# Kernel tuning notes

Measured on AMD Instinct MI355X. Metric: run time of the kernel, lower is better.

The kernel has to match this reference:

```python
import jax, jax.numpy as jnp
import numpy as np
import math

B, S = 2, 2048
IN_FEATURES = 4096
OUT_FEATURES = 4096
BLOCK_SIZE = 64
NUM_FFT_MATRICES = 4
IN_BLOCKS = IN_FEATURES // BLOCK_SIZE
OUT_BLOCKS = OUT_FEATURES // BLOCK_SIZE  # 64


def setup_inputs() -> dict:
    key = jax.random.key(0)
    k1, k2 = jax.random.split(key)
    scale = 1.0 / math.sqrt(BLOCK_SIZE * IN_BLOCKS)
    x = jax.random.normal(k1, (B, S, IN_FEATURES), dtype=jnp.float32)
    circulant_params = jax.random.normal(
        k2, (NUM_FFT_MATRICES, OUT_BLOCKS, IN_BLOCKS, BLOCK_SIZE), dtype=jnp.float32) * scale
    channel_weights = jnp.ones((NUM_FFT_MATRICES,), dtype=jnp.float32) / NUM_FFT_MATRICES
    return {"x": x, "circulant_params": circulant_params, "channel_weights": channel_weights}


def reference(x, circulant_params, channel_weights):
    b, s, in_feat = x.shape
    # split channels into circulant blocks: (b, s, in_blocks, block)
    x_blocks = x.reshape(b, s, IN_BLOCKS, BLOCK_SIZE)
    x_fft = jnp.fft.rfft(x_blocks, axis=-1)                    # (b, s, i, F) complex
    circ_fft = jnp.fft.rfft(circulant_params, axis=-1)         # (m, o, i, F) complex
    # channel-weighted combine over the m fft matrices (linear, so fold into weights)
    circ_w = jnp.einsum('m,moif->oif', channel_weights.astype(circ_fft.dtype), circ_fft)
    # per-frequency complex contraction over in_blocks (the block-circulant matmul)
    y_fft = jnp.einsum('bsif,oif->bsof', x_fft, circ_w)        # (b, s, o, F)
    y = jnp.fft.irfft(y_fft, n=BLOCK_SIZE, axis=-1)            # (b, s, o, block)
    return y.reshape(b, s, OUT_FEATURES).astype(x.dtype)
```

## Files before the change

kernel.cpp:

```cpp
#include <hip/hip_runtime.h>
#include <math.h>


typedef unsigned short u16;
typedef unsigned int   u32;
typedef __attribute__((ext_vector_type(8))) short bf16x8;
typedef __attribute__((ext_vector_type(4))) float f32x4;

#define TWO_PI 6.2831853071795864769f
#define SLICE 262144u

#define XF_ELEMS (33u * 2u * SLICE)
#define BF_OFF   XF_ELEMS
#define BF_ELEMS (33u * 128u * 128u)
#define DT_OFF   (BF_OFF + BF_ELEMS)
#define DT_ELEMS (2u * 80u * 40u)
#define E_OFF    (DT_OFF + DT_ELEMS)
#define E_ELEMS  (64u * 3u * 40u)

__device__ __forceinline__ u16 f2bf(float f) {
    union { float f; unsigned u; } v; v.f = f;
    unsigned r = v.u + 0x7FFFu + ((v.u >> 16) & 1u);
    return (u16)(r >> 16);
}

__global__ void prep(const float* __restrict__ p, const float* __restrict__ cw,
                     u16* __restrict__ Bf, u16* __restrict__ Dt, u16* __restrict__ E) {
    const int tid = threadIdx.x;
    if (blockIdx.x == 0) {
        for (int e = tid; e < (int)DT_ELEMS; e += 256) {
            int kt = e / 3200, rem = e % 3200, n = rem / 40, kk = rem % 40;
            int k = kt * 32 + kk;
            float v = 0.f;
            if (n < 66 && kk < 32) {
                int f = n >> 1;
                float ang = TWO_PI * (float)((f * k) & 63) * (1.f / 64.f);
                v = (n & 1) ? -sinf(ang) : cosf(ang);
            }
            Dt[e] = f2bf(v);
        }
        for (int e = tid; e < (int)E_ELEMS; e += 256) {
            int t = e / 120, rem = e % 120, kt = rem / 40, kk = rem % 40;
            int k = kt * 32 + kk;
            float v = 0.f;
            if (k < 66 && kk < 32) {
                int f = k >> 1;
                float wf = (f == 0 || f == 32) ? 1.f : 2.f;
                float ang = TWO_PI * (float)((f * t) & 63) * (1.f / 64.f);
                v = (wf * (1.f / 64.f)) * ((k & 1) ? -sinf(ang) : cosf(ang));
            }
            E[e] = f2bf(v);
        }
        return;
    }
    __shared__ float  ct[4][64];
    __shared__ float2 trig[64];
    const int pr = tid >> 6, ln = tid & 63;
    if (tid < 64) {
        float s, c;
        sincosf(TWO_PI * (float)tid * (1.f / 64.f), &s, &c);
        trig[tid] = make_float2(s, c);
    }
    const int pg = (blockIdx.x - 1) * 4 + pr;
    const int o = pg >> 6, i = pg & 63;
    {
        const float* base = p + (size_t)o * 4096 + i * 64 + ln;
        ct[pr][ln] = cw[0] * base[0]      + cw[1] * base[262144]
                   + cw[2] * base[524288] + cw[3] * base[786432];
    }
    __syncthreads();
    if (ln < 33) {
        float cr = 0.f, ci = 0.f;
        for (int u = 0; u < 64; ++u) {
            float2 sc = trig[(ln * u) & 63];
            cr += ct[pr][u] * sc.y; ci -= ct[pr][u] * sc.x;
        }
        u16* b = Bf + (size_t)ln * 16384 + (2 * o) * 128 + 2 * i;
        b[0]   = f2bf(cr);  b[1]   = f2bf(-ci);
        b[128] = f2bf(ci);  b[129] = f2bf(cr);
    }
}

__global__ __launch_bounds__(256) void t1_dft(const float* __restrict__ x,
                                              const u16* __restrict__ Dt,
                                              u16* __restrict__ XF) {
    __shared__ u32 TR[33 * 4 * 68];
    const int tid = threadIdx.x, lane = tid & 63, wave = tid >> 6;
    const int lm = lane & 15, kq8 = (lane >> 4) * 8;
    const int blk = blockIdx.x;
    const float* xb = x + (size_t)blk * 16384;

    f32x4 acc[4][5];
#pragma unroll
    for (int mi = 0; mi < 4; ++mi)
#pragma unroll
        for (int ni = 0; ni < 5; ++ni) acc[mi][ni] = (f32x4){0.f, 0.f, 0.f, 0.f};

#pragma unroll
    for (int kt = 0; kt < 2; ++kt) {
        bf16x8 bfr[5];
#pragma unroll
        for (int ni = 0; ni < 5; ++ni)
            bfr[ni] = *(const bf16x8*)&Dt[(kt * 80 + ni * 16 + lm) * 40 + kq8];
#pragma unroll
        for (int mi = 0; mi < 4; ++mi) {
            const int row = wave * 64 + mi * 16 + lm;
            const float* rp = xb + row * 64 + kt * 32 + kq8;
            float4 p0 = *(const float4*)rp;
            float4 p1 = *(const float4*)(rp + 4);
            union { u16 u[8]; bf16x8 v; } pk;
            pk.u[0] = f2bf(p0.x); pk.u[1] = f2bf(p0.y);
            pk.u[2] = f2bf(p0.z); pk.u[3] = f2bf(p0.w);
            pk.u[4] = f2bf(p1.x); pk.u[5] = f2bf(p1.y);
            pk.u[6] = f2bf(p1.z); pk.u[7] = f2bf(p1.w);
#pragma unroll
            for (int ni = 0; ni < 5; ++ni)
                acc[mi][ni] = __builtin_amdgcn_mfma_f32_16x16x32_bf16(
                    pk.v, bfr[ni], acc[mi][ni], 0, 0, 0);
        }
    }

    const int r0 = (lane >> 4) * 4;
#pragma unroll
    for (int mi = 0; mi < 4; ++mi)
#pragma unroll
        for (int ni = 0; ni < 5; ++ni) {
            const int col = ni * 16 + lm;
            if (col < 66) {
                const int f = col >> 1, par = col & 1;
                const int rowb = wave * 64 + mi * 16 + r0;
                f32x4 v = acc[mi][ni];
#pragma unroll
                for (int r = 0; r < 4; ++r) {
                    int rr = rowb + r, tokl = rr >> 6, ii = rr & 63;
                    ((u16*)TR)[(f * 272 + tokl * 68 + ii) * 2 + par] = f2bf(v[r]);
                }
            }
        }
    __syncthreads();
    u32* XFu = (u32*)XF;
#pragma unroll
    for (int rnd = 0; rnd < 9; ++rnd) {
        int s = rnd * 16 + wave * 4 + (lane >> 4);
        if (s < 132) {
            int f = s >> 2, tokl = s & 3, c = lm * 4;
            uint4 v = *(const uint4*)&TR[f * 272 + tokl * 68 + c];
            *(uint4*)&XFu[(size_t)f * SLICE + (size_t)(blk * 4 + tokl) * 64 + c] = v;
        }
    }
}

#define GLD(g, l) __builtin_amdgcn_global_load_lds(                         \
        (const __attribute__((address_space(1))) void*)(g),                 \
        (__attribute__((address_space(3))) void*)(l), 16, 0, 0)

__global__ __launch_bounds__(256) void t2_freq(u16* __restrict__ XF,
                                               const u16* __restrict__ Bf) {
    __shared__ u16 sA[128 * 32];
    __shared__ u16 sB[128 * 32];
    const int f = blockIdx.y;
    u16* XFf = XF + (size_t)f * (2u * SLICE);
    const u16* Bff = Bf + (size_t)f * 16384;
    const int tid = threadIdx.x, lane = tid & 63, wid = tid >> 6;
    const int wm = wid >> 1, wn = wid & 1;
    const int lm = lane & 15, kq = (lane >> 4) * 8;
    const int tileM = blockIdx.x * 128;

    f32x4 acc[4][4];
#pragma unroll
    for (int i = 0; i < 4; ++i)
#pragma unroll
        for (int j = 0; j < 4; ++j) acc[i][j] = (f32x4){0.f, 0.f, 0.f, 0.f};

    const int e0 = tid * 8, e1 = 2048 + tid * 8;
    const u16* gA0 = XFf + (size_t)(tileM + (e0 >> 5)) * 128 + (e0 & 31);
    const u16* gA1 = XFf + (size_t)(tileM + (e1 >> 5)) * 128 + (e1 & 31);
    const u16* gB0 = Bff + (size_t)(e0 >> 5) * 128 + (e0 & 31);
    const u16* gB1 = Bff + (size_t)(e1 >> 5) * 128 + (e1 & 31);
    u16* lA0 = &sA[wid * 512];
    u16* lA1 = &sA[2048 + wid * 512];
    u16* lB0 = &sB[wid * 512];
    u16* lB1 = &sB[2048 + wid * 512];

#pragma unroll
    for (int kt = 0; kt < 128; kt += 32) {
        __syncthreads();
        GLD(gA0 + kt, lA0);
        GLD(gA1 + kt, lA1);
        GLD(gB0 + kt, lB0);
        GLD(gB1 + kt, lB1);
        __syncthreads();
        bf16x8 af[4], bfr[4];
#pragma unroll
        for (int mi = 0; mi < 4; ++mi)
            af[mi] = *(const bf16x8*)&sA[(wm * 64 + mi * 16 + lm) * 32 + kq];
#pragma unroll
        for (int ni = 0; ni < 4; ++ni)
            bfr[ni] = *(const bf16x8*)&sB[(wn * 64 + ni * 16 + lm) * 32 + kq];
#pragma unroll
        for (int mi = 0; mi < 4; ++mi)
#pragma unroll
            for (int ni = 0; ni < 4; ++ni)
                acc[mi][ni] = __builtin_amdgcn_mfma_f32_16x16x32_bf16(
                    af[mi], bfr[ni], acc[mi][ni], 0, 0, 0);
    }

    const int r0 = (lane >> 4) * 4;
#pragma unroll
    for (int mi = 0; mi < 4; ++mi)
#pragma unroll
        for (int ni = 0; ni < 4; ++ni) {
            const int row = tileM + wm * 64 + mi * 16 + r0;
            const int col = wn * 64 + ni * 16 + lm;
            f32x4 v = acc[mi][ni];
#pragma unroll
            for (int r = 0; r < 4; ++r)
                XFf[(size_t)(row + r) * 128 + col] = f2bf(v[r]);
        }
}

__global__ __launch_bounds__(256) void t3_idft(const u16* __restrict__ YF,
                                               const u16* __restrict__ E,
                                               float* __restrict__ y) {
    __shared__ u16 sA[3 * 128 * 40];
    __shared__ u16 sE[64 * 120];
    const int tid = threadIdx.x, lane = tid & 63, wave = tid >> 6;
    u32* sA32 = (u32*)sA;
#pragma unroll
    for (int j = 0; j < 4; ++j) {
        int e = j * 256 + tid;
        int kt = e >> 9, row = (e >> 2) & 127, w = e & 3;
        sA32[kt * 2560 + row * 20 + 8 + w] = 0u;
    }
#pragma unroll
    for (int j = 0; j < 10; ++j)
        sA32[5120 + j * 256 + tid] = 0u;
    {
        const u32* src = (const u32*)E;
#pragma unroll
        for (int j = 0; j < 15; ++j)
            ((u32*)sE)[j * 256 + tid] = src[j * 256 + tid];
    }
    __syncthreads();
    const int tok0 = blockIdx.x * 2;
    const u32* YFu = (const u32*)YF;
#pragma unroll
    for (int j = 0; j < 17; ++j) {
        int e = j * 256 + tid;
        if (e < 4224) {
            int seg = e >> 6, o = e & 63;
            int f = seg >> 1, tokl = seg & 1;
            u32 v = YFu[(size_t)f * SLICE + (size_t)(tok0 + tokl) * 64 + o];
            int k = 2 * f;
            *(u32*)&sA[(k >> 5) * 5120 + (tokl * 64 + o) * 40 + (k & 31)] = v;
        }
    }
    __syncthreads();
    const int lm = lane & 15, kq8 = (lane >> 4) * 8;
    f32x4 acc[2][4];
#pragma unroll
    for (int mi = 0; mi < 2; ++mi)
#pragma unroll
        for (int ni = 0; ni < 4; ++ni) acc[mi][ni] = (f32x4){0.f, 0.f, 0.f, 0.f};
#pragma unroll
    for (int kt = 0; kt < 3; ++kt) {
        bf16x8 af[2], bfr[4];
#pragma unroll
        for (int mi = 0; mi < 2; ++mi)
            af[mi] = *(const bf16x8*)&sA[kt * 5120 + (wave * 32 + mi * 16 + lm) * 40 + kq8];
#pragma unroll
        for (int ni = 0; ni < 4; ++ni)
            bfr[ni] = *(const bf16x8*)&sE[(ni * 16 + lm) * 120 + kt * 40 + kq8];
#pragma unroll
        for (int mi = 0; mi < 2; ++mi)
#pragma unroll
            for (int ni = 0; ni < 4; ++ni)
                acc[mi][ni] = __builtin_amdgcn_mfma_f32_16x16x32_bf16(
                    af[mi], bfr[ni], acc[mi][ni], 0, 0, 0);
    }
    const int r0 = (lane >> 4) * 4;
#pragma unroll
    for (int mi = 0; mi < 2; ++mi)
#pragma unroll
        for (int ni = 0; ni < 4; ++ni) {
            int row = blockIdx.x * 128 + wave * 32 + mi * 16 + r0;
            int t = ni * 16 + lm;
            f32x4 v = acc[mi][ni];
#pragma unroll
            for (int r = 0; r < 4; ++r)
                y[(size_t)(row + r) * 64 + t] = v[r];
        }
}

extern "C" void kernel_launch(void* const* d_in, const int* in_sizes, int n_in,
                              void* d_out, int out_size, void* d_ws, size_t ws_size,
                              hipStream_t stream) {
    const float* x      = (const float*)d_in[0];
    const float* params = (const float*)d_in[1];
    const float* cw     = (const float*)d_in[2];
    float* out = (float*)d_out;

    u16* XF = (u16*)d_ws;
    u16* Bf = XF + BF_OFF;
    u16* Dt = XF + DT_OFF;
    u16* Eg = XF + E_OFF;

    prep<<<1025, 256, 0, stream>>>(params, cw, Bf, Dt, Eg);
    t1_dft<<<1024, 256, 0, stream>>>(x, Dt, XF);
    t2_freq<<<dim3(32, 33), 256, 0, stream>>>(XF, Bf);
    t3_idft<<<2048, 256, 0, stream>>>(XF, Eg, out);
}
```

Baseline: 170.2 us.

## Fuse forward DFT, frequency contraction and inverse DFT into one kernel

Replaces the three-kernel pipeline (DFT, per-frequency GEMM, inverse DFT) with a single 512-thread kernel. Each block keeps 16 tokens' frequency data in shared memory using an XOR-swizzled layout, so the large XF intermediate no longer goes through global memory. The goal is to remove the intermediate global write and read traffic and two launches. In exchange, only 256 blocks run with about 135KB of LDS each, which limits occupancy. The Bf weights are read straight from global (L2) per wave rather than staged through LDS.

```diff
diff --git a/kernel.cpp b/kernel.cpp
--- a/kernel.cpp
+++ b/kernel.cpp
@@ -8,15 +8,13 @@
 typedef __attribute__((ext_vector_type(4))) float f32x4;
 
 #define TWO_PI 6.2831853071795864769f
-#define SLICE 262144u
-
-#define XF_ELEMS (33u * 2u * SLICE)
-#define BF_OFF   XF_ELEMS
-#define BF_ELEMS (33u * 128u * 128u)
-#define DT_OFF   (BF_OFF + BF_ELEMS)
-#define DT_ELEMS (2u * 80u * 40u)
+
+#define SF 2056
+#define BF_ELEMS (33u*128u*128u)
+#define DT_OFF   BF_ELEMS
+#define DT_ELEMS (2u*4u*80u*8u)
 #define E_OFF    (DT_OFF + DT_ELEMS)
-#define E_ELEMS  (64u * 3u * 40u)
+#define E_ELEMS  (3u*4u*64u*8u)
 
 __device__ __forceinline__ u16 f2bf(float f) {
     union { float f; unsigned u; } v; v.f = f;
@@ -29,10 +27,11 @@
     const int tid = threadIdx.x;
     if (blockIdx.x == 0) {
         for (int e = tid; e < (int)DT_ELEMS; e += 256) {
-            int kt = e / 3200, rem = e % 3200, n = rem / 40, kk = rem % 40;
-            int k = kt * 32 + kk;
+            int j = e & 7, rowid = e >> 3;
+            int n = rowid % 80, grp = rowid / 80;
+            int k = (grp >> 2) * 32 + (grp & 3) * 8 + j;
             float v = 0.f;
-            if (n < 66 && kk < 32) {
+            if (n < 66) {
                 int f = n >> 1;
                 float ang = TWO_PI * (float)((f * k) & 63) * (1.f / 64.f);
                 v = (n & 1) ? -sinf(ang) : cosf(ang);
@@ -40,10 +39,11 @@
             Dt[e] = f2bf(v);
         }
         for (int e = tid; e < (int)E_ELEMS; e += 256) {
-            int t = e / 120, rem = e % 120, kt = rem / 40, kk = rem % 40;
-            int k = kt * 32 + kk;
+            int j = e & 7, rowid = e >> 3;
+            int t = rowid % 64, grp = rowid / 64;
+            int k = (grp >> 2) * 32 + (grp & 3) * 8 + j;
             float v = 0.f;
-            if (k < 66 && kk < 32) {
+            if (k < 66) {
                 int f = k >> 1;
                 float wf = (f == 0 || f == 32) ? 1.f : 2.f;
                 float ang = TWO_PI * (float)((f * t) & 63) * (1.f / 64.f);
@@ -81,215 +81,125 @@
     }
 }
 
-__global__ __launch_bounds__(256) void t1_dft(const float* __restrict__ x,
-                                              const u16* __restrict__ Dt,
-                                              u16* __restrict__ XF) {
-    __shared__ u32 TR[33 * 4 * 68];
+__global__ __launch_bounds__(512) void fused(const float* __restrict__ x,
+                                             const u16* __restrict__ Dt,
+                                             const u16* __restrict__ Bf,
+                                             const u16* __restrict__ E2,
+                                             float* __restrict__ y) {
+    __shared__ u16 sm[33 * SF];
     const int tid = threadIdx.x, lane = tid & 63, wave = tid >> 6;
-    const int lm = lane & 15, kq8 = (lane >> 4) * 8;
-    const int blk = blockIdx.x;
-    const float* xb = x + (size_t)blk * 16384;
-
-    f32x4 acc[4][5];
-#pragma unroll
-    for (int mi = 0; mi < 4; ++mi)
-#pragma unroll
-        for (int ni = 0; ni < 5; ++ni) acc[mi][ni] = (f32x4){0.f, 0.f, 0.f, 0.f};
-
-#pragma unroll
-    for (int kt = 0; kt < 2; ++kt) {
-        bf16x8 bfr[5];
-#pragma unroll
-        for (int ni = 0; ni < 5; ++ni)
-            bfr[ni] = *(const bf16x8*)&Dt[(kt * 80 + ni * 16 + lm) * 40 + kq8];
-#pragma unroll
-        for (int mi = 0; mi < 4; ++mi) {
-            const int row = wave * 64 + mi * 16 + lm;
-            const float* rp = xb + row * 64 + kt * 32 + kq8;
-            float4 p0 = *(const float4*)rp;
-            float4 p1 = *(const float4*)(rp + 4);
-            union { u16 u[8]; bf16x8 v; } pk;
-            pk.u[0] = f2bf(p0.x); pk.u[1] = f2bf(p0.y);
-            pk.u[2] = f2bf(p0.z); pk.u[3] = f2bf(p0.w);
-            pk.u[4] = f2bf(p1.x); pk.u[5] = f2bf(p1.y);
-            pk.u[6] = f2bf(p1.z); pk.u[7] = f2bf(p1.w);
+    const int lm = lane & 15, q = lane >> 4, kq8 = q * 8, r0 = q * 4;
+    const float* xb = x + (size_t)blockIdx.x * (16u * 4096u);
+
+#pragma unroll
+    for (int pass = 0; pass < 2; ++pass) {
+        f32x4 acc[4][5];
+#pragma unroll
+        for (int mi = 0; mi < 4; ++mi)
+#pragma unroll
+            for (int ni = 0; ni < 5; ++ni) acc[mi][ni] = (f32x4){0.f,0.f,0.f,0.f};
+#pragma unroll
+        for (int kt = 0; kt < 2; ++kt) {
+            bf16x8 bfr[5];
 #pragma unroll
             for (int ni = 0; ni < 5; ++ni)
-                acc[mi][ni] = __builtin_amdgcn_mfma_f32_16x16x32_bf16(
-                    pk.v, bfr[ni], acc[mi][ni], 0, 0, 0);
-        }
-    }
-
-    const int r0 = (lane >> 4) * 4;
-#pragma unroll
-    for (int mi = 0; mi < 4; ++mi)
-#pragma unroll
-        for (int ni = 0; ni < 5; ++ni) {
-            const int col = ni * 16 + lm;
-            if (col < 66) {
-                const int f = col >> 1, par = col & 1;
-                const int rowb = wave * 64 + mi * 16 + r0;
-                f32x4 v = acc[mi][ni];
-#pragma unroll
-                for (int r = 0; r < 4; ++r) {
-                    int rr = rowb + r, tokl = rr >> 6, ii = rr & 63;
-                    ((u16*)TR)[(f * 272 + tokl * 68 + ii) * 2 + par] = f2bf(v[r]);
+                bfr[ni] = *(const bf16x8*)&Dt[((kt*4 + q)*80 + ni*16 + lm)*8];
+#pragma unroll
+            for (int mi = 0; mi < 4; ++mi) {
+                const int row = wave*128 + pass*64 + mi*16 + lm;
+                const float* rp = xb + row*64 + kt*32 + kq8;
+                float4 p0 = *(const float4*)rp;
+                float4 p1 = *(const float4*)(rp + 4);
+                union { u16 u[8]; bf16x8 v; } pk;
+                pk.u[0]=f2bf(p0.x); pk.u[1]=f2bf(p0.y);
+                pk.u[2]=f2bf(p0.z); pk.u[3]=f2bf(p0.w);
+                pk.u[4]=f2bf(p1.x); pk.u[5]=f2bf(p1.y);
+                pk.u[6]=f2bf(p1.z); pk.u[7]=f2bf(p1.w);
+#pragma unroll
+                for (int ni = 0; ni < 5; ++ni)
+                    acc[mi][ni] = __builtin_amdgcn_mfma_f32_16x16x32_bf16(
+                        pk.v, bfr[ni], acc[mi][ni], 0, 0, 0);
+            }
+        }
+#pragma unroll
+        for (int mi = 0; mi < 4; ++mi)
+#pragma unroll
+            for (int ni = 0; ni < 5; ++ni) {
+                const int col = ni*16 + lm;
+                if (col < 66) {
+                    const int f = col >> 1, par = col & 1;
+                    const int mb = wave*128 + pass*64 + mi*16 + r0;
+                    f32x4 v = acc[mi][ni];
+#pragma unroll
+                    for (int r = 0; r < 4; ++r) {
+                        int m = mb + r, tok = m >> 6, ii = m & 63;
+                        sm[f*SF + tok*128 + (((ii<<1)|par) ^ ((tok&7)<<3))] = f2bf(v[r]);
+                    }
                 }
             }
-        }
+    }
     __syncthreads();
-    u32* XFu = (u32*)XF;
-#pragma unroll
-    for (int rnd = 0; rnd < 9; ++rnd) {
-        int s = rnd * 16 + wave * 4 + (lane >> 4);
-        if (s < 132) {
-            int f = s >> 2, tokl = s & 3, c = lm * 4;
-            uint4 v = *(const uint4*)&TR[f * 272 + tokl * 68 + c];
-            *(uint4*)&XFu[(size_t)f * SLICE + (size_t)(blk * 4 + tokl) * 64 + c] = v;
-        }
-    }
-}
-
-#define GLD(g, l) __builtin_amdgcn_global_load_lds(                         \
-        (const __attribute__((address_space(1))) void*)(g),                 \
-        (__attribute__((address_space(3))) void*)(l), 16, 0, 0)
-
-__global__ __launch_bounds__(256) void t2_freq(u16* __restrict__ XF,
-                                               const u16* __restrict__ Bf) {
-    __shared__ u16 sA[128 * 32];
-    __shared__ u16 sB[128 * 32];
-    const int f = blockIdx.y;
-    u16* XFf = XF + (size_t)f * (2u * SLICE);
-    const u16* Bff = Bf + (size_t)f * 16384;
-    const int tid = threadIdx.x, lane = tid & 63, wid = tid >> 6;
-    const int wm = wid >> 1, wn = wid & 1;
-    const int lm = lane & 15, kq = (lane >> 4) * 8;
-    const int tileM = blockIdx.x * 128;
-
-    f32x4 acc[4][4];
-#pragma unroll
-    for (int i = 0; i < 4; ++i)
-#pragma unroll
-        for (int j = 0; j < 4; ++j) acc[i][j] = (f32x4){0.f, 0.f, 0.f, 0.f};
-
-    const int e0 = tid * 8, e1 = 2048 + tid * 8;
-    const u16* gA0 = XFf + (size_t)(tileM + (e0 >> 5)) * 128 + (e0 & 31);
-    const u16* gA1 = XFf + (size_t)(tileM + (e1 >> 5)) * 128 + (e1 & 31);
-    const u16* gB0 = Bff + (size_t)(e0 >> 5) * 128 + (e0 & 31);
-    const u16* gB1 = Bff + (size_t)(e1 >> 5) * 128 + (e1 & 31);
-    u16* lA0 = &sA[wid * 512];
-    u16* lA1 = &sA[2048 + wid * 512];
-    u16* lB0 = &sB[wid * 512];
-    u16* lB1 = &sB[2048 + wid * 512];
-
-#pragma unroll
-    for (int kt = 0; kt < 128; kt += 32) {
-        __syncthreads();
-        GLD(gA0 + kt, lA0);
-        GLD(gA1 + kt, lA1);
-        GLD(gB0 + kt, lB0);
-        GLD(gB1 + kt, lB1);
-        __syncthreads();
-        bf16x8 af[4], bfr[4];
-#pragma unroll
-        for (int mi = 0; mi < 4; ++mi)
-            af[mi] = *(const bf16x8*)&sA[(wm * 64 + mi * 16 + lm) * 32 + kq];
-#pragma unroll
-        for (int ni = 0; ni < 4; ++ni)
-            bfr[ni] = *(const bf16x8*)&sB[(wn * 64 + ni * 16 + lm) * 32 + kq];
-#pragma unroll
-        for (int mi = 0; mi < 4; ++mi)
-#pragma unroll
-            for (int ni = 0; ni < 4; ++ni)
-                acc[mi][ni] = __builtin_amdgcn_mfma_f32_16x16x32_bf16(
-                    af[mi], bfr[ni], acc[mi][ni], 0, 0, 0);
-    }
-
-    const int r0 = (lane >> 4) * 4;
-#pragma unroll
-    for (int mi = 0; mi < 4; ++mi)
-#pragma unroll
-        for (int ni = 0; ni < 4; ++ni) {
-            const int row = tileM + wm * 64 + mi * 16 + r0;
-            const int col = wn * 64 + ni * 16 + lm;
-            f32x4 v = acc[mi][ni];
-#pragma unroll
-            for (int r = 0; r < 4; ++r)
-                XFf[(size_t)(row + r) * 128 + col] = f2bf(v[r]);
-        }
-}
-
-__global__ __launch_bounds__(256) void t3_idft(const u16* __restrict__ YF,
-                                               const u16* __restrict__ E,
-                                               float* __restrict__ y) {
-    __shared__ u16 sA[3 * 128 * 40];
-    __shared__ u16 sE[64 * 120];
-    const int tid = threadIdx.x, lane = tid & 63, wave = tid >> 6;
-    u32* sA32 = (u32*)sA;
-#pragma unroll
-    for (int j = 0; j < 4; ++j) {
-        int e = j * 256 + tid;
-        int kt = e >> 9, row = (e >> 2) & 127, w = e & 3;
-        sA32[kt * 2560 + row * 20 + 8 + w] = 0u;
-    }
-#pragma unroll
-    for (int j = 0; j < 10; ++j)
-        sA32[5120 + j * 256 + tid] = 0u;
-    {
-        const u32* src = (const u32*)E;
-#pragma unroll
-        for (int j = 0; j < 15; ++j)
-            ((u32*)sE)[j * 256 + tid] = src[j * 256 + tid];
+
+    for (int f = wave; f < 33; f += 8) {
+        u16* sl = &sm[f * SF];
+        const u16* Bff = Bf + (size_t)f * 16384;
+        bf16x8 af[4];
+#pragma unroll
+        for (int ks = 0; ks < 4; ++ks)
+            af[ks] = *(const bf16x8*)&sl[lm*128 + ((ks*32 + kq8) ^ ((lm&7)<<3))];
+#pragma unroll
+        for (int nt = 0; nt < 8; ++nt) {
+            f32x4 c = (f32x4){0.f,0.f,0.f,0.f};
+#pragma unroll
+            for (int ks = 0; ks < 4; ++ks) {
+                bf16x8 bq = *(const bf16x8*)&Bff[(nt*16 + lm)*128 + ks*32 + kq8];
+                c = __builtin_amdgcn_mfma_f32_16x16x32_bf16(af[ks], bq, c, 0, 0, 0);
+            }
+#pragma unroll
+            for (int r = 0; r < 4; ++r) {
+                int tok = r0 + r;
+                sl[tok*128 + ((nt*16 + lm) ^ ((tok&7)<<3))] = f2bf(c[r]);
+            }
+        }
     }
     __syncthreads();
-    const int tok0 = blockIdx.x * 2;
-    const u32* YFu = (const u32*)YF;
-#pragma unroll
-    for (int j = 0; j < 17; ++j) {
-        int e = j * 256 + tid;
-        if (e < 4224) {
-            int seg = e >> 6, o = e & 63;
-            int f = seg >> 1, tokl = seg & 1;
-            u32 v = YFu[(size_t)f * SLICE + (size_t)(tok0 + tokl) * 64 + o];
-            int k = 2 * f;
-            *(u32*)&sA[(k >> 5) * 5120 + (tokl * 64 + o) * 40 + (k & 31)] = v;
-        }
-    }
-    __syncthreads();
-    const int lm = lane & 15, kq8 = (lane >> 4) * 8;
-    f32x4 acc[2][4];
-#pragma unroll
-    for (int mi = 0; mi < 2; ++mi)
-#pragma unroll
-        for (int ni = 0; ni < 4; ++ni) acc[mi][ni] = (f32x4){0.f, 0.f, 0.f, 0.f};
-#pragma unroll
-    for (int kt = 0; kt < 3; ++kt) {
-        bf16x8 af[2], bfr[4];
-#pragma unroll
-        for (int mi = 0; mi < 2; ++mi)
-            af[mi] = *(const bf16x8*)&sA[kt * 5120 + (wave * 32 + mi * 16 + lm) * 40 + kq8];
-#pragma unroll
-        for (int ni = 0; ni < 4; ++ni)
-            bfr[ni] = *(const bf16x8*)&sE[(ni * 16 + lm) * 120 + kt * 40 + kq8];
-#pragma unroll
-        for (int mi = 0; mi < 2; ++mi)
-#pragma unroll
-            for (int ni = 0; ni < 4; ++ni)
-                acc[mi][ni] = __builtin_amdgcn_mfma_f32_16x16x32_bf16(
-                    af[mi], bfr[ni], acc[mi][ni], 0, 0, 0);
-    }
-    const int r0 = (lane >> 4) * 4;
-#pragma unroll
-    for (int mi = 0; mi < 2; ++mi)
-#pragma unroll
-        for (int ni = 0; ni < 4; ++ni) {
-            int row = blockIdx.x * 128 + wave * 32 + mi * 16 + r0;
-            int t = ni * 16 + lm;
-            f32x4 v = acc[mi][ni];
-#pragma unroll
-            for (int r = 0; r < 4; ++r)
-                y[(size_t)(row + r) * 64 + t] = v[r];
-        }
+
+    bf16x8 ef[3][4];
+#pragma unroll
+    for (int kt = 0; kt < 3; ++kt)
+#pragma unroll
+        for (int mt = 0; mt < 4; ++mt)
+            ef[kt][mt] = *(const bf16x8*)&E2[((kt*4 + q)*64 + mt*16 + lm)*8];
+#pragma unroll
+    for (int nt = 0; nt < 8; ++nt) {
+        const int tokL = wave*2 + (nt >> 2);
+        const int o = (nt & 3)*16 + lm;
+        const int cb = tokL*128 + ((2*o) ^ ((tokL&7)<<3));
+        f32x4 acc[4];
+#pragma unroll
+        for (int mt = 0; mt < 4; ++mt) acc[mt] = (f32x4){0.f,0.f,0.f,0.f};
+#pragma unroll
+        for (int kt = 0; kt < 3; ++kt) {
+            union { u32 w[4]; bf16x8 v; } bq;
+#pragma unroll
+            for (int j = 0; j < 4; ++j) {
+                int f = kt*16 + q*4 + j;
+                u32 vv = 0u;
+                if (f < 33) vv = *(const u32*)&sm[f*SF + cb];
+                bq.w[j] = vv;
+            }
+#pragma unroll
+            for (int mt = 0; mt < 4; ++mt)
+                acc[mt] = __builtin_amdgcn_mfma_f32_16x16x32_bf16(
+                    ef[kt][mt], bq.v, acc[mt], 0, 0, 0);
+        }
+        float* yb = y + ((size_t)(blockIdx.x*16 + tokL))*4096 + o*64;
+#pragma unroll
+        for (int mt = 0; mt < 4; ++mt) {
+            float4 st = { acc[mt][0], acc[mt][1], acc[mt][2], acc[mt][3] };
+            *(float4*)&yb[mt*16 + r0] = st;
+        }
+    }
 }
 
 extern "C" void kernel_launch(void* const* d_in, const int* in_sizes, int n_in,
@@ -300,13 +210,10 @@
     const float* cw     = (const float*)d_in[2];
     float* out = (float*)d_out;
 
-    u16* XF = (u16*)d_ws;
-    u16* Bf = XF + BF_OFF;
-    u16* Dt = XF + DT_OFF;
-    u16* Eg = XF + E_OFF;
+    u16* Bf = (u16*)d_ws;
+    u16* Dt = Bf + DT_OFF;
+    u16* Eg = Bf + E_OFF;
 
     prep<<<1025, 256, 0, stream>>>(params, cw, Bf, Dt, Eg);
-    t1_dft<<<1024, 256, 0, stream>>>(x, Dt, XF);
-    t2_freq<<<dim3(32, 33), 256, 0, stream>>>(XF, Bf);
-    t3_idft<<<2048, 256, 0, stream>>>(XF, Eg, out);
-}
+    fused<<<256, 512, 0, stream>>>(x, Dt, Bf, Eg, out);
+}
```

Result: faster. 161.7 us (-5.0%).
